# Performance work log

Measured on AMD Instinct MI355X. Metric: run time of the kernel, lower is better.

## Reference

```python
import jax, jax.numpy as jnp
import numpy as np

B, IN_SEQ, HID_SEQ, OUT_SEQ = 2, 2048, 2048, 2048
C_IN, C_OUT, H = 1024, 1024, 16
HD = C_OUT // H  # 64


def _linear_params(key, out_f, in_f):
    kw, kb = jax.random.split(key)
    bound = 1.0 / np.sqrt(in_f)
    w = jax.random.uniform(kw, (out_f, in_f), jnp.float32, -bound, bound)
    b = jax.random.uniform(kb, (out_f,), jnp.float32, -bound, bound)
    return w, b


def setup_inputs() -> dict:
    key = jax.random.key(0)
    ks = jax.random.split(key, 6)
    x = jax.random.normal(ks[0], (B, IN_SEQ, C_IN), jnp.float32)
    w_hseq, b_hseq = _linear_params(ks[1], HID_SEQ, IN_SEQ)
    wq, bq = _linear_params(ks[2], C_OUT, C_IN)
    wk, bk = _linear_params(ks[3], C_OUT, C_IN)
    wv, bv = _linear_params(ks[4], C_OUT, C_IN)
    w_oseq, b_oseq = _linear_params(ks[5], OUT_SEQ, HID_SEQ)
    return {"x": x, "w_hseq": w_hseq, "b_hseq": b_hseq,
            "wq": wq, "bq": bq, "wk": wk, "bk": bk, "wv": wv, "bv": bv,
            "w_oseq": w_oseq, "b_oseq": b_oseq}


def reference(x, w_hseq, b_hseq, wq, bq, wk, bk, wv, bv, w_oseq, b_oseq):
    b = x.shape[0]
    # seq-axis projection: Linear(in_seq -> hidden_seq) applied to x.transpose(1,2)
    # xh[b, t, c] = sum_s x[b, s, c] * w_hseq[t, s] + b_hseq[t]
    xh = jnp.einsum('bsc,ts->btc', x, w_hseq) + b_hseq[:, None]
    q = (xh @ wq.T + bq).reshape(b, HID_SEQ, H, HD).transpose(0, 2, 1, 3)  # [B,H,Sh,hd]
    k = (xh @ wk.T + bk).reshape(b, HID_SEQ, H, HD).transpose(0, 2, 1, 3)
    v = (xh @ wv.T + bv).reshape(b, HID_SEQ, H, HD).transpose(0, 2, 1, 3)
    scores = jnp.einsum('bhqd,bhkd->bhqk', q, k) / np.sqrt(HD).astype(np.float32)
    attn = jax.nn.softmax(scores, axis=-1)                       # [B,H,Sh,Sh]
    flex = jnp.einsum('bhqk,ok->bhqo', attn, w_oseq) + b_oseq    # [B,H,Sh,So]
    # flexscale.transpose(-2,-1) @ v contracts over the QUERY axis q
    out = jnp.einsum('bhqo,bhqd->bhod', flex, v)                 # [B,H,So,hd]
    return out.transpose(0, 2, 1, 3).reshape(b, OUT_SEQ, C_OUT)
```

## Files before the change

### kernel.cpp

```cpp
#include <hip/hip_runtime.h>
#include <hip/hip_bf16.h>

typedef unsigned short u16;
typedef unsigned int u32;
typedef unsigned long long u64;
typedef __attribute__((ext_vector_type(8))) short s16x8;
typedef __attribute__((ext_vector_type(4))) float f32x4;
typedef __attribute__((ext_vector_type(16))) float f32x16;

#define SCL 0.1803368867f

#if __has_builtin(__builtin_amdgcn_exp2f)
#define EXP2(x) __builtin_amdgcn_exp2f(x)
#else
#define EXP2(x) exp2f(x)
#endif

__device__ __forceinline__ float bf2f(u16 v){ u32 u = ((u32)v)<<16; return __builtin_bit_cast(float,u); }
__device__ __forceinline__ u16 f2bf(float f){
  u32 u = __builtin_bit_cast(u32,f);
  u += 0x7fff + ((u>>16)&1);
  return (u16)(u>>16);
}
__device__ __forceinline__ u32 pkbf(float a, float b){
  u32 ua = __builtin_bit_cast(u32,a) + 0x8000u;
  u32 ub = __builtin_bit_cast(u32,b) + 0x8000u;
  return (ua>>16) | (ub & 0xFFFF0000u);
}
__device__ __forceinline__ void glds16(const u16* g, const u16* lds_u){
  __builtin_amdgcn_global_load_lds(
      (const __attribute__((address_space(1))) void*)(u64)g,
      (__attribute__((address_space(3))) void*)(u32)(u64)lds_u,
      16, 0, 0);
}
__device__ __forceinline__ f32x4 mfma16(s16x8 a, s16x8 b, f32x4 c){
  return __builtin_amdgcn_mfma_f32_16x16x32_bf16(a,b,c,0,0,0);
}

__global__ __launch_bounds__(256) void detect_dtype(const u16* __restrict__ x, u32* __restrict__ flag){
  __shared__ int cnt;
  if (threadIdx.x==0) cnt = 0;
  __syncthreads();
  int local = 0;
  for (int i = threadIdx.x; i < 4096; i += 256){
    u16 v = x[2*i];
    int e = (v>>7)&0xFF;
    if (e >= 140 || e <= 100) local++;
  }
  atomicAdd(&cnt, local);
  __syncthreads();
  if (threadIdx.x==0) *flag = (cnt > 1024) ? 1u : 0u;
}

struct CvtArgs { const void* src[11]; u16* dst[11]; int n[11]; };

__global__ __launch_bounds__(256) void convert_inputs(CvtArgs a, const u32* __restrict__ flag){
  const int which = blockIdx.y;
  const int n = a.n[which];
  const int base = blockIdx.x*2048 + threadIdx.x;
  if (base >= n) return;
  u16* dst = a.dst[which];
  if (*flag){
    const float* s = (const float*)a.src[which];
    #pragma unroll
    for (int j=0;j<8;j++){ int i = base + j*256; if (i<n) dst[i] = f2bf(s[i]); }
  } else {
    const u16* s = (const u16*)a.src[which];
    #pragma unroll
    for (int j=0;j<8;j++){ int i = base + j*256; if (i<n) dst[i] = s[i]; }
  }
}

__global__ __launch_bounds__(256) void transpose_k(
    const u16* __restrict__ src, u16* __restrict__ dst,
    int ldS, long srcBatch, long dstBatch, int colOff)
{
  __shared__ u16 T[64][72];
  const int s0 = blockIdx.x*64, c0 = blockIdx.y*64, b = blockIdx.z;
  const int t = threadIdx.x;
  {
    const int r = t>>2, cc = (t&3)*16;
    const u16* p = src + (long)b*srcBatch + (long)(s0+r)*ldS + colOff + c0 + cc;
    *(s16x8*)&T[r][cc]   = *(const s16x8*)p;
    *(s16x8*)&T[r][cc+8] = *(const s16x8*)(p+8);
  }
  __syncthreads();
  {
    const int orow = t&63, oc = (t>>6)*16;
    u16 tmp[16];
    #pragma unroll
    for (int j=0;j<16;j++) tmp[j] = T[oc+j][orow];
    u16* q = dst + (long)b*dstBatch + (long)(c0+orow)*2048 + s0 + oc;
    *(s16x8*)q     = *(s16x8*)&tmp[0];
    *(s16x8*)(q+8) = *(s16x8*)&tmp[8];
  }
}

__global__ __launch_bounds__(256) void transpose_scale_k(
    const u16* __restrict__ qkv, const float* __restrict__ lS, u16* __restrict__ dst)
{
  __shared__ u16 T[64][72];
  __shared__ float ils[64];
  const int s0 = blockIdx.x*64, c0 = blockIdx.y*64, b = blockIdx.z;
  const int t = threadIdx.x;
  if (t < 64) ils[t] = lS[((long)(b*16 + (c0>>6)))*2048 + s0 + t];
  __syncthreads();
  {
    const int r = t>>2, cc = (t&3)*16;
    const u16* p = qkv + (long)b*6291456 + (long)(s0+r)*3072 + 2048 + c0 + cc;
    const float sc = ils[r];
    s16x8 v0 = *(const s16x8*)p, v1 = *(const s16x8*)(p+8);
    #pragma unroll
    for (int j=0;j<8;j++){
      T[r][cc+j]   = f2bf(bf2f((u16)v0[j])*sc);
      T[r][cc+8+j] = f2bf(bf2f((u16)v1[j])*sc);
    }
  }
  __syncthreads();
  {
    const int orow = t&63, oc = (t>>6)*16;
    u16 tmp[16];
    #pragma unroll
    for (int j=0;j<16;j++) tmp[j] = T[oc+j][orow];
    u16* q = dst + (long)b*2097152 + (long)(c0+orow)*2048 + s0 + oc;
    *(s16x8*)q     = *(s16x8*)&tmp[0];
    *(s16x8*)(q+8) = *(s16x8*)&tmp[8];
  }
}

__global__ __launch_bounds__(256) void rowsum_part(const u16* __restrict__ qkv, float* __restrict__ svp){
  const int c = blockIdx.x*256 + threadIdx.x;
  const int b = c>>10, cc = c&1023;
  const int tz = blockIdx.y;
  const u16* p = qkv + ((long)(b*2048 + tz*256))*3072 + 2048 + cc;
  float s = 0.f;
  #pragma unroll 8
  for (int i=0;i<256;i++) s += bf2f(p[(long)i*3072]);
  svp[tz*2048 + c] = s;
}
__global__ __launch_bounds__(256) void rowsum_fin(const float* __restrict__ svp, float* __restrict__ sv){
  const int c = blockIdx.x*256 + threadIdx.x;
  float s = 0.f;
  #pragma unroll
  for (int z=0;z<8;z++) s += svp[z*2048 + c];
  sv[c] = s;
}

template<int BN, int BMODE, bool DYN, bool QS>
__global__ __launch_bounds__(256) void gemm_t(
    const u16* __restrict__ A, const u16* __restrict__ B,
    const u16* __restrict__ bias, const float* __restrict__ r1col,
    const u32* __restrict__ dflag, void* __restrict__ C,
    int K, int lda, int ldb, int ldc,
    long aBatch, long bBatch, long cBatch)
{
  constexpr int BM = 128;
  constexpr int ACH = BM/64, BCH = BN/64;
  constexpr int MI = (BN==128) ? 4 : 2;
  __shared__ u16 As[2][BM*32];
  __shared__ u16 Bs[2][BN*32];
  const int t = threadIdx.x, w = t>>6, quad = (t&63)>>4, l16 = t&15;
  const int z = blockIdx.z;
  const int m0 = blockIdx.x*BM, n0 = blockIdx.y*BN;
  const u16* Ag = A + (long)z*aBatch + (long)m0*lda;
  const u16* Bg = B + (long)z*bBatch + (long)n0*ldb;
  const int wm = (BN==128) ? (w>>1)*64 : w*32;
  const int wn = (BN==128) ? (w&1)*64 : 0;

  auto stage = [&](int buf, int k0){
    #pragma unroll
    for (int i=0;i<ACH;i++){
      const int chunk = i*256 + t;
      glds16(Ag + (long)(chunk>>2)*lda + k0 + (chunk&3)*8, &As[buf][(i*256 + w*64)*8]);
    }
    #pragma unroll
    for (int i=0;i<BCH;i++){
      const int chunk = i*256 + t;
      glds16(Bg + (long)(chunk>>2)*ldb + k0 + (chunk&3)*8, &Bs[buf][(i*256 + w*64)*8]);
    }
  };

  f32x4 acc[MI][4];
  #pragma unroll
  for (int i=0;i<MI;i++)
    #pragma unroll
    for (int j=0;j<4;j++) acc[i][j] = (f32x4){0.f,0.f,0.f,0.f};

  stage(0, 0);
  const int nk = K>>5;
  for (int kt=0; kt<nk; ++kt){
    __syncthreads();
    if (kt+1 < nk) stage((kt+1)&1, (kt+1)<<5);
    const u16* as = As[kt&1];
    const u16* bs = Bs[kt&1];
    s16x8 a[MI], bb[4];
    #pragma unroll
    for (int i=0;i<MI;i++) a[i] = *(const s16x8*)&as[(wm + i*16 + l16)*32 + quad*8];
    #pragma unroll
    for (int j=0;j<4;j++)  bb[j]= *(const s16x8*)&bs[(wn + j*16 + l16)*32 + quad*8];
    #pragma unroll
    for (int i=0;i<MI;i++)
      #pragma unroll
      for (int j=0;j<4;j++)
        acc[i][j] = mfma16(a[i], bb[j], acc[i][j]);
  }

  bool f32o = false;
  if (DYN) f32o = (*dflag != 0);
  #pragma unroll
  for (int i=0;i<MI;i++){
    #pragma unroll
    for (int j=0;j<4;j++){
      const int col = n0 + wn + j*16 + l16;
      #pragma unroll
      for (int r=0;r<4;r++){
        const int row = m0 + wm + i*16 + quad*4 + r;
        float vv = acc[i][j][r];
        if (BMODE==1) vv += bf2f(bias[row]);
        if (BMODE==2) vv += bf2f(bias[col]);
        if (BMODE==3) vv += bf2f(bias[row]) * r1col[z*1024 + col];
        if (QS){ if (col < 1024) vv *= SCL; }
        const long idx = (long)z*cBatch + (long)row*ldc + col;
        if (DYN && f32o) ((float*)C)[idx] = vv;
        else             ((u16*)C)[idx]   = f2bf(vv);
      }
    }
  }
}

__global__ __launch_bounds__(256) void attn_stats(const u16* __restrict__ qkv, float* __restrict__ lS){
  __shared__ u16 Qs[64][68];
  __shared__ u16 Ks[64][68];
  __shared__ float red[2][64];
  const int q0 = blockIdx.x*64, bh = blockIdx.y, b = bh>>4, h = bh&15;
  const int t = threadIdx.x, w = t>>6, l32 = t&31, half = (t&63)>>5;
  const int wq = w>>1, wk = w&1;
  {
    const int r = t>>2, cc = (t&3)*16;
    const u16* p = &qkv[((long)(b*2048 + q0 + r))*3072 + h*64 + cc];
    *(s16x8*)&Qs[r][cc]   = *(const s16x8*)p;
    *(s16x8*)&Qs[r][cc+8] = *(const s16x8*)(p+8);
  }
  __syncthreads();
  s16x8 aq[4];
  #pragma unroll
  for (int u=0;u<4;u++) aq[u] = *(s16x8*)&Qs[wq*32 + l32][u*16 + half*8];
  float lp[16];
  #pragma unroll
  for (int r=0;r<16;r++) lp[r] = 0.f;

  for (int kc=0; kc<2048; kc+=64){
    __syncthreads();
    {
      const int r = t>>2, cc = (t&3)*16;
      const u16* p = &qkv[((long)(b*2048 + kc + r))*3072 + 1024 + h*64 + cc];
      *(s16x8*)&Ks[r][cc]   = *(const s16x8*)p;
      *(s16x8*)&Ks[r][cc+8] = *(const s16x8*)(p+8);
    }
    __syncthreads();
    s16x8 kb[4];
    #pragma unroll
    for (int u=0;u<4;u++) kb[u] = *(s16x8*)&Ks[wk*32 + l32][u*16 + half*8];
    f32x16 acc = {};
    #pragma unroll
    for (int u=0;u<4;u++) acc = __builtin_amdgcn_mfma_f32_32x32x16_bf16(aq[u], kb[u], acc, 0,0,0);
    #pragma unroll
    for (int r=0;r<16;r++) lp[r] += EXP2(acc[r]);
  }
  #pragma unroll
  for (int off=1; off<32; off<<=1)
    #pragma unroll
    for (int r=0;r<16;r++) lp[r] += __shfl_xor(lp[r], off);
  if (l32 == 0){
    #pragma unroll
    for (int r=0;r<16;r++)
      red[wk][wq*32 + 4*half + (r&3) + 8*(r>>2)] = lp[r];
  }
  __syncthreads();
  if (t < 64){
    float l = red[0][t] + red[1][t];
    lS[(long)bh*2048 + q0 + t] = 1.f/l;
  }
}

__global__ __launch_bounds__(256) void attn_pv(
    const u16* __restrict__ qkv, const u16* __restrict__ VtG, u16* __restrict__ Mt)
{
  __shared__ u16 Ks[64][68];
  __shared__ u16 Qs[64][68];
  __shared__ u16 Vs[64][68];
  __shared__ u16 Ps[64][68];
  const int k0 = blockIdx.x*64, bh = blockIdx.y, b = bh>>4, h = bh&15;
  const int t = threadIdx.x, w = t>>6, l32 = t&31, half = (t&63)>>5;
  const int wr = w>>1, wk = w&1;
  {
    const int r = t>>2, cc = (t&3)*16;
    const u16* p = &qkv[((long)(b*2048 + k0 + r))*3072 + 1024 + h*64 + cc];
    *(s16x8*)&Ks[r][cc]   = *(const s16x8*)p;
    *(s16x8*)&Ks[r][cc+8] = *(const s16x8*)(p+8);
  }
  __syncthreads();
  s16x8 kb[4];
  #pragma unroll
  for (int u=0;u<4;u++) kb[u] = *(s16x8*)&Ks[wk*32 + l32][u*16 + half*8];

  f32x16 accM = {};
  for (int q0=0; q0<2048; q0+=64){
    __syncthreads();
    {
      const int r = t>>2, cc = (t&3)*16;
      const u16* pq = &qkv[((long)(b*2048 + q0 + r))*3072 + h*64 + cc];
      *(s16x8*)&Qs[r][cc]   = *(const s16x8*)pq;
      *(s16x8*)&Qs[r][cc+8] = *(const s16x8*)(pq+8);
      const u16* pv = &VtG[((long)(b*1024 + h*64 + r))*2048 + q0 + cc];
      *(s16x8*)&Vs[r][cc]   = *(const s16x8*)pv;
      *(s16x8*)&Vs[r][cc+8] = *(const s16x8*)(pv+8);
    }
    __syncthreads();
    s16x8 aq[4];
    #pragma unroll
    for (int u=0;u<4;u++) aq[u] = *(s16x8*)&Qs[wr*32 + l32][u*16 + half*8];
    f32x16 acc = {};
    #pragma unroll
    for (int u=0;u<4;u++) acc = __builtin_amdgcn_mfma_f32_32x32x16_bf16(aq[u], kb[u], acc, 0,0,0);
    const int kcol = wk*32 + l32;
    #pragma unroll
    for (int g=0; g<4; g++){
      float p0 = EXP2(acc[4*g+0]);
      float p1 = EXP2(acc[4*g+1]);
      float p2 = EXP2(acc[4*g+2]);
      float p3 = EXP2(acc[4*g+3]);
      u64 v = (u64)pkbf(p0,p1) | ((u64)pkbf(p2,p3) << 32);
      *(u64*)&Ps[kcol][wr*32 + 8*g + 4*half] = v;
    }
    __syncthreads();
    s16x8 av[4], bp[4];
    #pragma unroll
    for (int u=0;u<4;u++) av[u] = *(s16x8*)&Vs[wr*32 + l32][u*16 + half*8];
    #pragma unroll
    for (int u=0;u<4;u++) bp[u] = *(s16x8*)&Ps[wk*32 + l32][u*16 + half*8];
    #pragma unroll
    for (int u=0;u<4;u++) accM = __builtin_amdgcn_mfma_f32_32x32x16_bf16(av[u], bp[u], accM, 0,0,0);
  }
  #pragma unroll
  for (int r=0;r<16;r++){
    const int d = wr*32 + 4*half + (r&3) + 8*(r>>2);
    const int k = k0 + wk*32 + l32;
    Mt[((long)(b*1024 + h*64 + d))*2048 + k] = f2bf(accM[r]);
  }
}

extern "C" void kernel_launch(void* const* d_in, const int* in_sizes, int n_in,
                              void* d_out, int out_size, void* d_ws, size_t ws_size,
                              hipStream_t stream)
{
  (void)n_in; (void)out_size; (void)ws_size;
  char* ws = (char*)d_ws;
  u32*  dflag = (u32*)ws;            ws += 64;
  u16*  xc    = (u16*)ws;            ws += (size_t)8388608;
  u16*  whc   = (u16*)ws;            ws += (size_t)8388608;
  u16*  wqkvc = (u16*)ws;            ws += (size_t)6291456;
  u16*  woc   = (u16*)ws;            ws += (size_t)8388608;
  u16*  bhc   = (u16*)ws;            ws += 4096;
  u16*  bqkvc = (u16*)ws;            ws += 8192;
  u16*  boc   = (u16*)ws;            ws += 4096;
  u16*  xT    = (u16*)ws;            ws += (size_t)8388608;
  u16*  xh    = (u16*)ws;            ws += (size_t)8388608;
  u16*  qkvb  = (u16*)ws;            ws += (size_t)25165824;
  u16*  VtG   = (u16*)ws;            ws += (size_t)8388608;
  u16*  Mt    = (u16*)ws;            ws += (size_t)8388608;
  float* lS   = (float*)ws;          ws += (size_t)262144;
  float* svp  = (float*)ws;          ws += (size_t)65536;
  float* sv   = (float*)ws;          ws += 8192;

  detect_dtype<<<1,256,0,stream>>>((const u16*)d_in[0], dflag);
  CvtArgs ca;
  u16* dsts[11] = {xc, whc, bhc, wqkvc, bqkvc, wqkvc+1048576, bqkvc+1024,
                   wqkvc+2097152, bqkvc+2048, woc, boc};
  for (int i=0;i<11;i++){ ca.src[i]=d_in[i]; ca.dst[i]=dsts[i]; ca.n[i]=in_sizes[i]; }
  convert_inputs<<<dim3(2048,11),256,0,stream>>>(ca, dflag);

  const long S2M = 2097152L;

  transpose_k<<<dim3(32,16,2),256,0,stream>>>(xc, xT, 1024, S2M, S2M, 0);

  gemm_t<64,1,false,false><<<dim3(16,16,2),256,0,stream>>>(whc, xT, bhc, nullptr, dflag, xh,
      2048, 2048, 2048, 1024, 0L, S2M, S2M);

  gemm_t<128,2,false,true><<<dim3(16,24,2),256,0,stream>>>(xh, wqkvc, bqkvc, nullptr, dflag, qkvb,
      1024, 1024, 1024, 3072, S2M, 0L, (long)2048*3072);

  rowsum_part<<<dim3(8,8),256,0,stream>>>(qkvb, svp);
  rowsum_fin<<<8,256,0,stream>>>(svp, sv);

  attn_stats<<<dim3(32,32),256,0,stream>>>(qkvb, lS);

  transpose_scale_k<<<dim3(32,16,2),256,0,stream>>>(qkvb, lS, VtG);

  attn_pv<<<dim3(32,32),256,0,stream>>>(qkvb, VtG, Mt);

  gemm_t<64,3,true,false><<<dim3(16,16,2),256,0,stream>>>(woc, Mt, boc, sv, dflag, d_out,
      2048, 2048, 2048, 1024, 0L, S2M, S2M);
}
```

Measured before the change: 357.5 us.

## Use 32x32 MFMA with swizzled LDS in GEMM and register-resident P in attn_pv

The generic GEMM moves from 16x16x32 to 32x32x16 bf16 MFMA tiles and XOR-swizzles the 16-byte chunks staged into LDS to cut bank conflicts on fragment reads. attn_pv stops writing the exponentiated scores to LDS and reading them back after a barrier. Instead it rearranges them in registers with cross-half shuffles into B operands, and each warp accumulates a partial over its query slice. The two row-warps' partials are then reduced through an LDS scratch area at the end. This removes a barrier and the P round trip per iteration, at the cost of extra shuffles, twice the accumulator registers and a final reduction.

```diff
diff --git a/kernel.cpp b/kernel.cpp
--- a/kernel.cpp
+++ b/kernel.cpp
@@ -33,8 +33,8 @@
       (__attribute__((address_space(3))) void*)(u32)(u64)lds_u,
       16, 0, 0);
 }
-__device__ __forceinline__ f32x4 mfma16(s16x8 a, s16x8 b, f32x4 c){
-  return __builtin_amdgcn_mfma_f32_16x16x32_bf16(a,b,c,0,0,0);
+__device__ __forceinline__ f32x16 mfma32(s16x8 a, s16x8 b, f32x16 c){
+  return __builtin_amdgcn_mfma_f32_32x32x16_bf16(a,b,c,0,0,0);
 }
 
 __global__ __launch_bounds__(256) void detect_dtype(const u16* __restrict__ x, u32* __restrict__ flag){
@@ -155,36 +155,50 @@
     long aBatch, long bBatch, long cBatch)
 {
   constexpr int BM = 128;
-  constexpr int ACH = BM/64, BCH = BN/64;
-  constexpr int MI = (BN==128) ? 4 : 2;
+  constexpr int ACH = 2, BCH = BN/64;
+  constexpr int NI = (BN==128) ? 2 : 1;
   __shared__ u16 As[2][BM*32];
   __shared__ u16 Bs[2][BN*32];
-  const int t = threadIdx.x, w = t>>6, quad = (t&63)>>4, l16 = t&15;
+  const int t = threadIdx.x, w = t>>6, l32 = t&31, half = (t&63)>>5;
   const int z = blockIdx.z;
   const int m0 = blockIdx.x*BM, n0 = blockIdx.y*BN;
   const u16* Ag = A + (long)z*aBatch + (long)m0*lda;
   const u16* Bg = B + (long)z*bBatch + (long)n0*ldb;
-  const int wm = (BN==128) ? (w>>1)*64 : w*32;
-  const int wn = (BN==128) ? (w&1)*64 : 0;
+  const int wm = (w>>1)*64;
+  const int wn = (BN==128) ? (w&1)*64 : (w&1)*32;
 
   auto stage = [&](int buf, int k0){
     #pragma unroll
     for (int i=0;i<ACH;i++){
-      const int chunk = i*256 + t;
-      glds16(Ag + (long)(chunk>>2)*lda + k0 + (chunk&3)*8, &As[buf][(i*256 + w*64)*8]);
+      const int chunk = i*256 + t, row = chunk>>2;
+      const int cg = (chunk&3) ^ (row&3);
+      glds16(Ag + (long)row*lda + k0 + cg*8, &As[buf][(i*256 + w*64)*8]);
     }
     #pragma unroll
     for (int i=0;i<BCH;i++){
-      const int chunk = i*256 + t;
-      glds16(Bg + (long)(chunk>>2)*ldb + k0 + (chunk&3)*8, &Bs[buf][(i*256 + w*64)*8]);
+      const int chunk = i*256 + t, row = chunk>>2;
+      const int cg = (chunk&3) ^ (row&3);
+      glds16(Bg + (long)row*ldb + k0 + cg*8, &Bs[buf][(i*256 + w*64)*8]);
     }
   };
 
-  f32x4 acc[MI][4];
-  #pragma unroll
-  for (int i=0;i<MI;i++)
-    #pragma unroll
-    for (int j=0;j<4;j++) acc[i][j] = (f32x4){0.f,0.f,0.f,0.f};
+  int aoff[2][2], boff[NI][2];
+  #pragma unroll
+  for (int mi=0; mi<2; mi++)
+    #pragma unroll
+    for (int kc=0; kc<2; kc++){
+      const int row = wm + mi*32 + l32;
+      aoff[mi][kc] = row*32 + ((kc*2+half) ^ (row&3))*8;
+    }
+  #pragma unroll
+  for (int ni=0; ni<NI; ni++)
+    #pragma unroll
+    for (int kc=0; kc<2; kc++){
+      const int row = wn + ni*32 + l32;
+      boff[ni][kc] = row*32 + ((kc*2+half) ^ (row&3))*8;
+    }
+
+  f32x16 acc[2][NI] = {};
 
   stage(0, 0);
   const int nk = K>>5;
@@ -193,29 +207,35 @@
     if (kt+1 < nk) stage((kt+1)&1, (kt+1)<<5);
     const u16* as = As[kt&1];
     const u16* bs = Bs[kt&1];
-    s16x8 a[MI], bb[4];
-    #pragma unroll
-    for (int i=0;i<MI;i++) a[i] = *(const s16x8*)&as[(wm + i*16 + l16)*32 + quad*8];
-    #pragma unroll
-    for (int j=0;j<4;j++)  bb[j]= *(const s16x8*)&bs[(wn + j*16 + l16)*32 + quad*8];
-    #pragma unroll
-    for (int i=0;i<MI;i++)
-      #pragma unroll
-      for (int j=0;j<4;j++)
-        acc[i][j] = mfma16(a[i], bb[j], acc[i][j]);
+    s16x8 a[2][2], bb[NI][2];
+    #pragma unroll
+    for (int mi=0;mi<2;mi++)
+      #pragma unroll
+      for (int kc=0;kc<2;kc++) a[mi][kc] = *(const s16x8*)&as[aoff[mi][kc]];
+    #pragma unroll
+    for (int ni=0;ni<NI;ni++)
+      #pragma unroll
+      for (int kc=0;kc<2;kc++) bb[ni][kc] = *(const s16x8*)&bs[boff[ni][kc]];
+    #pragma unroll
+    for (int kc=0;kc<2;kc++)
+      #pragma unroll
+      for (int mi=0;mi<2;mi++)
+        #pragma unroll
+        for (int ni=0;ni<NI;ni++)
+          acc[mi][ni] = mfma32(a[mi][kc], bb[ni][kc], acc[mi][ni]);
   }
 
   bool f32o = false;
   if (DYN) f32o = (*dflag != 0);
   #pragma unroll
-  for (int i=0;i<MI;i++){
-    #pragma unroll
-    for (int j=0;j<4;j++){
-      const int col = n0 + wn + j*16 + l16;
-      #pragma unroll
-      for (int r=0;r<4;r++){
-        const int row = m0 + wm + i*16 + quad*4 + r;
-        float vv = acc[i][j][r];
+  for (int mi=0;mi<2;mi++){
+    #pragma unroll
+    for (int ni=0;ni<NI;ni++){
+      const int col = n0 + wn + ni*32 + l32;
+      #pragma unroll
+      for (int r=0;r<16;r++){
+        const int row = m0 + wm + mi*32 + (r&3) + 8*(r>>2) + 4*half;
+        float vv = acc[mi][ni][r];
         if (BMODE==1) vv += bf2f(bias[row]);
         if (BMODE==2) vv += bf2f(bias[col]);
         if (BMODE==3) vv += bf2f(bias[row]) * r1col[z*1024 + col];
@@ -263,7 +283,7 @@
     for (int u=0;u<4;u++) kb[u] = *(s16x8*)&Ks[wk*32 + l32][u*16 + half*8];
     f32x16 acc = {};
     #pragma unroll
-    for (int u=0;u<4;u++) acc = __builtin_amdgcn_mfma_f32_32x32x16_bf16(aq[u], kb[u], acc, 0,0,0);
+    for (int u=0;u<4;u++) acc = mfma32(aq[u], kb[u], acc);
     #pragma unroll
     for (int r=0;r<16;r++) lp[r] += EXP2(acc[r]);
   }
@@ -286,67 +306,88 @@
 __global__ __launch_bounds__(256) void attn_pv(
     const u16* __restrict__ qkv, const u16* __restrict__ VtG, u16* __restrict__ Mt)
 {
-  __shared__ u16 Ks[64][68];
-  __shared__ u16 Qs[64][68];
-  __shared__ u16 Vs[64][68];
-  __shared__ u16 Ps[64][68];
+  __shared__ __align__(16) u16 SH[3*64*68];
+  u16* Ksp = SH;
+  u16* Qsp = SH + 64*68;
+  u16* Vsp = SH + 2*64*68;
+  float* scr = (float*)(SH + 64*68);
   const int k0 = blockIdx.x*64, bh = blockIdx.y, b = bh>>4, h = bh&15;
   const int t = threadIdx.x, w = t>>6, l32 = t&31, half = (t&63)>>5;
   const int wr = w>>1, wk = w&1;
   {
     const int r = t>>2, cc = (t&3)*16;
     const u16* p = &qkv[((long)(b*2048 + k0 + r))*3072 + 1024 + h*64 + cc];
-    *(s16x8*)&Ks[r][cc]   = *(const s16x8*)p;
-    *(s16x8*)&Ks[r][cc+8] = *(const s16x8*)(p+8);
+    *(s16x8*)&Ksp[r*68+cc]   = *(const s16x8*)p;
+    *(s16x8*)&Ksp[r*68+cc+8] = *(const s16x8*)(p+8);
   }
   __syncthreads();
   s16x8 kb[4];
   #pragma unroll
-  for (int u=0;u<4;u++) kb[u] = *(s16x8*)&Ks[wk*32 + l32][u*16 + half*8];
-
-  f32x16 accM = {};
+  for (int u=0;u<4;u++) kb[u] = *(s16x8*)&Ksp[(wk*32 + l32)*68 + u*16 + half*8];
+
+  f32x16 accM[2] = {};
   for (int q0=0; q0<2048; q0+=64){
     __syncthreads();
     {
       const int r = t>>2, cc = (t&3)*16;
       const u16* pq = &qkv[((long)(b*2048 + q0 + r))*3072 + h*64 + cc];
-      *(s16x8*)&Qs[r][cc]   = *(const s16x8*)pq;
-      *(s16x8*)&Qs[r][cc+8] = *(const s16x8*)(pq+8);
+      *(s16x8*)&Qsp[r*68+cc]   = *(const s16x8*)pq;
+      *(s16x8*)&Qsp[r*68+cc+8] = *(const s16x8*)(pq+8);
       const u16* pv = &VtG[((long)(b*1024 + h*64 + r))*2048 + q0 + cc];
-      *(s16x8*)&Vs[r][cc]   = *(const s16x8*)pv;
-      *(s16x8*)&Vs[r][cc+8] = *(const s16x8*)(pv+8);
+      *(s16x8*)&Vsp[r*68+cc]   = *(const s16x8*)pv;
+      *(s16x8*)&Vsp[r*68+cc+8] = *(const s16x8*)(pv+8);
     }
     __syncthreads();
     s16x8 aq[4];
     #pragma unroll
-    for (int u=0;u<4;u++) aq[u] = *(s16x8*)&Qs[wr*32 + l32][u*16 + half*8];
+    for (int u=0;u<4;u++) aq[u] = *(s16x8*)&Qsp[(wr*32 + l32)*68 + u*16 + half*8];
     f32x16 acc = {};
     #pragma unroll
-    for (int u=0;u<4;u++) acc = __builtin_amdgcn_mfma_f32_32x32x16_bf16(aq[u], kb[u], acc, 0,0,0);
-    const int kcol = wk*32 + l32;
-    #pragma unroll
-    for (int g=0; g<4; g++){
-      float p0 = EXP2(acc[4*g+0]);
-      float p1 = EXP2(acc[4*g+1]);
-      float p2 = EXP2(acc[4*g+2]);
-      float p3 = EXP2(acc[4*g+3]);
-      u64 v = (u64)pkbf(p0,p1) | ((u64)pkbf(p2,p3) << 32);
-      *(u64*)&Ps[kcol][wr*32 + 8*g + 4*half] = v;
-    }
-    __syncthreads();
-    s16x8 av[4], bp[4];
-    #pragma unroll
-    for (int u=0;u<4;u++) av[u] = *(s16x8*)&Vs[wr*32 + l32][u*16 + half*8];
-    #pragma unroll
-    for (int u=0;u<4;u++) bp[u] = *(s16x8*)&Ps[wk*32 + l32][u*16 + half*8];
-    #pragma unroll
-    for (int u=0;u<4;u++) accM = __builtin_amdgcn_mfma_f32_32x32x16_bf16(av[u], bp[u], accM, 0,0,0);
-  }
-  #pragma unroll
-  for (int r=0;r<16;r++){
-    const int d = wr*32 + 4*half + (r&3) + 8*(r>>2);
-    const int k = k0 + wk*32 + l32;
-    Mt[((long)(b*1024 + h*64 + d))*2048 + k] = f2bf(accM[r]);
+    for (int u=0;u<4;u++) acc = mfma32(aq[u], kb[u], acc);
+    float e[16];
+    #pragma unroll
+    for (int r=0;r<16;r++) e[r] = EXP2(acc[r]);
+    float b0[8], b1[8];
+    #pragma unroll
+    for (int j=0;j<4;j++){
+      float sxa = __shfl_xor(e[4+j], 32);
+      float sxb = __shfl_xor(e[j],   32);
+      b0[j]   = (half==0) ? e[j]  : sxa;
+      b0[4+j] = (half==0) ? sxb   : e[4+j];
+      float sxc = __shfl_xor(e[12+j], 32);
+      float sxd = __shfl_xor(e[8+j],  32);
+      b1[j]   = (half==0) ? e[8+j] : sxc;
+      b1[4+j] = (half==0) ? sxd    : e[12+j];
+    }
+    union { u32 u[4]; s16x8 v; } f0, f1;
+    #pragma unroll
+    for (int m=0;m<4;m++){ f0.u[m] = pkbf(b0[2*m], b0[2*m+1]); f1.u[m] = pkbf(b1[2*m], b1[2*m+1]); }
+    #pragma unroll
+    for (int m=0;m<2;m++){
+      s16x8 av0 = *(s16x8*)&Vsp[(m*32 + l32)*68 + wr*32 + half*8];
+      s16x8 av1 = *(s16x8*)&Vsp[(m*32 + l32)*68 + wr*32 + 16 + half*8];
+      accM[m] = mfma32(av0, f0.v, accM[m]);
+      accM[m] = mfma32(av1, f1.v, accM[m]);
+    }
+  }
+  __syncthreads();
+  if (wr == 1){
+    #pragma unroll
+    for (int m=0;m<2;m++)
+      #pragma unroll
+      for (int r=0;r<16;r++)
+        scr[wk*2048 + m*1024 + (r*2+half)*32 + l32] = accM[m][r];
+  }
+  __syncthreads();
+  if (wr == 0){
+    #pragma unroll
+    for (int m=0;m<2;m++)
+      #pragma unroll
+      for (int r=0;r<16;r++){
+        const int d = m*32 + (r&3) + 8*(r>>2) + 4*half;
+        float v = accM[m][r] + scr[wk*2048 + m*1024 + (r*2+half)*32 + l32];
+        Mt[((long)(b*1024 + h*64 + d))*2048 + k0 + wk*32 + l32] = f2bf(v);
+      }
   }
 }
 
```

New measurement: 508.6 us. 1.42x slower.
